# Performance work log

Measured on AMD Instinct MI355X. Metric: run time of the kernel, lower is better.

Reference implementation:

```python
import jax, jax.numpy as jnp
import numpy as np

B, C, H, W = 8, 256, 64, 64
EPS = 1e-5


def _mk_conv_bn(key, oc, ic):
    k = jax.random.split(key, 6)
    return dict(
        w=jax.random.normal(k[0], (oc, ic), jnp.float32) * 0.01,  # trunc-normal approx, stddev 0.01
        b=jnp.zeros((oc,), jnp.float32),
        s=jax.random.uniform(k[1], (oc,), jnp.float32, 0.5, 1.5),   # BN scale
        t=jax.random.normal(k[2], (oc,), jnp.float32) * 0.1,        # BN shift
        m=jax.random.normal(k[3], (oc,), jnp.float32) * 0.1,        # BN running mean
        v=jax.random.uniform(k[4], (oc,), jnp.float32, 0.5, 1.5),   # BN running var
    )


def setup_inputs() -> dict:
    key = jax.random.key(0)
    ks = jax.random.split(key, 6)
    d = {"x": jax.random.normal(ks[0], (B, C, H, W), jnp.float32)}
    for i, (oc, ic) in zip([1, 2, 3, 4], [(C // 8, C), (C // 8, C), (C // 2, C), (C, C // 2)]):
        p = _mk_conv_bn(ks[i], oc, ic)
        for name, val in p.items():
            d[f"{name}{i}"] = val
    d["gamma"] = jnp.asarray(0.5, jnp.float32)
    return d


def _cbn(x, w, b, s, t, m, v, relu=True):
    # conv1x1 + BatchNorm(eval) [+ ReLU]; dropout is identity at inference
    y = jnp.einsum('bchw,oc->bohw', x, w) + b[None, :, None, None]
    scale = (s / jnp.sqrt(v + EPS))[None, :, None, None]
    y = (y - m[None, :, None, None]) * scale + t[None, :, None, None]
    return jax.nn.relu(y) if relu else y


def _maxpool2(x):
    b, c, h, w = x.shape
    return x.reshape(b, c, h // 2, 2, w // 2, 2).max(axis=(3, 5))


def reference(x, w1, b1, s1, t1, m1, v1, w2, b2, s2, t2, m2, v2,
              w3, b3, s3, t3, m3, v3, w4, b4, s4, t4, m4, v4, gamma):
    b, c, h, w = x.shape
    f = _maxpool2(_cbn(x, w1, b1, s1, t1, m1, v1))   # (B, C/8, H/2, W/2)
    g = _cbn(x, w2, b2, s2, t2, m2, v2)              # (B, C/8, H, W)
    hh = _maxpool2(_cbn(x, w3, b3, s3, t3, m3, v3))  # (B, C/2, H/2, W/2)
    hw, hw4 = h * w, (h // 2) * (w // 2)
    f = f.reshape(b, c // 8, hw4).transpose(0, 2, 1)  # (B, HW/4, C/8)
    g = g.reshape(b, c // 8, hw)                      # (B, C/8, HW)
    s = jnp.einsum('bnk,bkm->bnm', f, g)              # (B, HW/4, HW)
    beta = jax.nn.softmax(s, axis=1)                  # softmax over dim=1, as in source
    hh = hh.reshape(b, c // 2, hw4)                   # (B, C/2, HW/4)
    o = jnp.einsum('bcn,bnm->bcm', hh, beta).reshape(b, c // 2, h, w)
    out = _cbn(o, w4, b4, s4, t4, m4, v4, relu=False)
    return gamma * out + x
```

## Files before the change

kernel.cpp:

```cpp
#include <hip/hip_runtime.h>
#include <hip/hip_bf16.h>

#define HW   4096
#define HW4  1024
#define EPS  1e-5f

typedef __attribute__((ext_vector_type(8))) short bf16x8;
typedef __attribute__((ext_vector_type(4))) float f32x4;

__device__ __forceinline__ short f2bs(float f) {
    union { float f; unsigned u; } v; v.f = f;
    unsigned r = v.u + 0x7FFFu + ((v.u >> 16) & 1u);
    return (short)(r >> 16);
}
__device__ __forceinline__ float bs2f(short s) {
    union { unsigned u; float f; } v; v.u = ((unsigned)(unsigned short)s) << 16;
    return v.f;
}
__device__ __forceinline__ int swz64(int r, int c) { return (r << 6) + ((c ^ (r & 7)) << 3); }
__device__ __forceinline__ int swz32(int r, int c) { return (r << 5) + ((c ^ (r & 3)) << 3); }

__global__ __launch_bounds__(256) void conv123_mfma(
    const float* __restrict__ x,
    const float* __restrict__ w1, const float* __restrict__ b1, const float* __restrict__ s1,
    const float* __restrict__ t1, const float* __restrict__ m1, const float* __restrict__ v1,
    const float* __restrict__ w2, const float* __restrict__ b2, const float* __restrict__ s2,
    const float* __restrict__ t2, const float* __restrict__ m2, const float* __restrict__ v2,
    const float* __restrict__ w3, const float* __restrict__ b3, const float* __restrict__ s3,
    const float* __restrict__ t3, const float* __restrict__ m3, const float* __restrict__ v3,
    short* __restrict__ y192)
{
    __shared__ __align__(16) short Wl[192 * 64];
    __shared__ __align__(16) short Xl[64 * 64];
    __shared__ float alB[192], beB[192];

    const int t = threadIdx.x;
    const int lane = t & 63, wv = t >> 6;
    const int quad = lane >> 4, l16 = lane & 15;
    const int bz = blockIdx.y;
    const int pBase = blockIdx.x * 64;

    if (t < 192) {
        int j = t;
        float pb, ps, ptv, pm, pv;
        if (j < 32)      { pb = b1[j]; ps = s1[j]; ptv = t1[j]; pm = m1[j]; pv = v1[j]; }
        else if (j < 64) { int c = j - 32; pb = b2[c]; ps = s2[c]; ptv = t2[c]; pm = m2[c]; pv = v2[c]; }
        else             { int c = j - 64; pb = b3[c]; ps = s3[c]; ptv = t3[c]; pm = m3[c]; pv = v3[c]; }
        float al = ps * rsqrtf(pv + EPS);
        alB[j] = al; beB[j] = (pb - pm) * al + ptv;
    }

    const f32x4 fzero = {0.f, 0.f, 0.f, 0.f};
    f32x4 acc[3][4];
    #pragma unroll
    for (int i = 0; i < 3; ++i)
        #pragma unroll
        for (int j = 0; j < 4; ++j) acc[i][j] = fzero;

    for (int k0 = 0; k0 < 256; k0 += 64) {
        #pragma unroll
        for (int i = 0; i < 3; ++i) {
            int oc = i * 64 + (t >> 2);
            int kb = (t & 3) * 16;
            const float* wp;
            if (oc < 32)      wp = w1 + oc * 256;
            else if (oc < 64) wp = w2 + (oc - 32) * 256;
            else              wp = w3 + (oc - 64) * 256;
            float4 a = *(const float4*)(wp + k0 + kb);
            float4 b = *(const float4*)(wp + k0 + kb + 4);
            float4 c = *(const float4*)(wp + k0 + kb + 8);
            float4 d = *(const float4*)(wp + k0 + kb + 12);
            bf16x8 lo, hi;
            lo[0]=f2bs(a.x); lo[1]=f2bs(a.y); lo[2]=f2bs(a.z); lo[3]=f2bs(a.w);
            lo[4]=f2bs(b.x); lo[5]=f2bs(b.y); lo[6]=f2bs(b.z); lo[7]=f2bs(b.w);
            hi[0]=f2bs(c.x); hi[1]=f2bs(c.y); hi[2]=f2bs(c.z); hi[3]=f2bs(c.w);
            hi[4]=f2bs(d.x); hi[5]=f2bs(d.y); hi[6]=f2bs(d.z); hi[7]=f2bs(d.w);
            *(bf16x8*)&Wl[swz64(oc, (kb >> 3))]     = lo;
            *(bf16x8*)&Wl[swz64(oc, (kb >> 3) + 1)] = hi;
        }
        {
            int pp = t & 63, k8 = t >> 6;
            float fv[16];
            #pragma unroll
            for (int i = 0; i < 16; ++i)
                fv[i] = x[((size_t)bz * 256 + k0 + k8 * 16 + i) * HW + pBase + pp];
            bf16x8 lo, hi;
            #pragma unroll
            for (int i = 0; i < 8; ++i) { lo[i] = f2bs(fv[i]); hi[i] = f2bs(fv[8 + i]); }
            *(bf16x8*)&Xl[swz64(pp, k8 * 2)]     = lo;
            *(bf16x8*)&Xl[swz64(pp, k8 * 2 + 1)] = hi;
        }
        __syncthreads();
        #pragma unroll
        for (int kk = 0; kk < 2; ++kk) {
            bf16x8 bfr[4];
            #pragma unroll
            for (int pt = 0; pt < 4; ++pt)
                bfr[pt] = *(const bf16x8*)&Xl[swz64(pt * 16 + l16, kk * 4 + quad)];
            #pragma unroll
            for (int tt = 0; tt < 3; ++tt) {
                bf16x8 afr = *(const bf16x8*)&Wl[swz64(wv * 48 + tt * 16 + l16, kk * 4 + quad)];
                #pragma unroll
                for (int pt = 0; pt < 4; ++pt)
                    acc[tt][pt] = __builtin_amdgcn_mfma_f32_16x16x32_bf16(afr, bfr[pt], acc[tt][pt], 0, 0, 0);
            }
        }
        __syncthreads();
    }

    #pragma unroll
    for (int tt = 0; tt < 3; ++tt) {
        #pragma unroll
        for (int r = 0; r < 4; ++r) {
            int oc = wv * 48 + tt * 16 + quad * 4 + r;
            float al = alB[oc], be = beB[oc];
            #pragma unroll
            for (int pt = 0; pt < 4; ++pt) {
                int p = pBase + pt * 16 + l16;
                float y = fmaxf(acc[tt][pt][r] * al + be, 0.f);
                y192[((size_t)bz * 192 + oc) * HW + p] = f2bs(y);
            }
        }
    }
}

__global__ __launch_bounds__(256) void pool_kernel(
    const short* __restrict__ y192, short* __restrict__ fbuf, short* __restrict__ hhbuf)
{
    int t  = blockIdx.x * 256 + threadIdx.x;
    int n  = t & 1023;
    int ch = (t >> 10) % 160;
    int bz = t / (1024 * 160);
    int ph = n >> 5, pw = n & 31;
    int j = (ch < 32) ? ch : (ch + 32);
    const short* src = y192 + ((size_t)bz * 192 + j) * HW + (ph * 2) * 64 + pw * 2;
    float v00 = bs2f(src[0]), v01 = bs2f(src[1]), v10 = bs2f(src[64]), v11 = bs2f(src[65]);
    float mx = fmaxf(fmaxf(v00, v01), fmaxf(v10, v11));
    short o = f2bs(mx);
    if (ch < 32) fbuf[((size_t)bz * 32 + ch) * HW4 + n]          = o;
    else         hhbuf[((size_t)bz * 128 + (ch - 32)) * HW4 + n] = o;
}

__global__ __launch_bounds__(256) void attn_mfma(
    const short* __restrict__ y192,
    const short* __restrict__ fbuf,
    const short* __restrict__ hhbuf,
    short* __restrict__ obuf)
{
    __shared__ __align__(16) short gTl[64 * 32];
    __shared__ __align__(16) short fTl[64 * 32];
    __shared__ __align__(16) short hhl[128 * 64];
    __shared__ __align__(16) short sTl[64 * 64];

    const int t = threadIdx.x;
    const int lane = t & 63, wv = t >> 6;
    const int quad = lane >> 4, l16 = lane & 15;
    const int bz = blockIdx.y;
    const int m0 = blockIdx.x * 64;
    const int ms = wv * 16;
    const f32x4 fzero = {0.f, 0.f, 0.f, 0.f};

    {
        int mm = t & 63, k8 = t >> 6;
        bf16x8 v;
        #pragma unroll
        for (int j = 0; j < 8; ++j)
            v[j] = y192[((size_t)bz * 192 + 32 + k8 * 8 + j) * HW + m0 + mm];
        *(bf16x8*)&gTl[swz32(mm, k8)] = v;
    }
    __syncthreads();
    bf16x8 bg = *(const bf16x8*)&gTl[swz32(ms + l16, quad)];

    float runmax = -1e30f, runsum = 0.f;
    f32x4 oacc[8];
    #pragma unroll
    for (int i = 0; i < 8; ++i) oacc[i] = fzero;

    for (int n0 = 0; n0 < 1024; n0 += 64) {
        __syncthreads();
        {
            int nn = t & 63, k8 = t >> 6;
            bf16x8 v;
            #pragma unroll
            for (int j = 0; j < 8; ++j)
                v[j] = fbuf[((size_t)bz * 32 + k8 * 8 + j) * HW4 + n0 + nn];
            *(bf16x8*)&fTl[swz32(nn, k8)] = v;
        }
        {
            int c0 = t >> 3, nc = t & 7;
            #pragma unroll
            for (int i = 0; i < 4; ++i) {
                int c = i * 32 + c0;
                bf16x8 v = *(const bf16x8*)(hhbuf + ((size_t)bz * 128 + c) * HW4 + n0 + nc * 8);
                *(bf16x8*)&hhl[swz64(c, nc)] = v;
            }
        }
        __syncthreads();

        f32x4 sacc[4];
        #pragma unroll
        for (int nt = 0; nt < 4; ++nt) {
            bf16x8 af = *(const bf16x8*)&fTl[swz32(nt * 16 + l16, quad)];
            sacc[nt] = __builtin_amdgcn_mfma_f32_16x16x32_bf16(af, bg, fzero, 0, 0, 0);
        }

        float tmax = -1e30f;
        #pragma unroll
        for (int nt = 0; nt < 4; ++nt)
            #pragma unroll
            for (int r = 0; r < 4; ++r) tmax = fmaxf(tmax, sacc[nt][r]);
        tmax = fmaxf(tmax, __shfl_xor(tmax, 16));
        tmax = fmaxf(tmax, __shfl_xor(tmax, 32));
        float nmax  = fmaxf(runmax, tmax);
        float alpha = __expf(runmax - nmax);
        float psum = 0.f;
        #pragma unroll
        for (int nt = 0; nt < 4; ++nt) {
            short4 ev;
            #pragma unroll
            for (int r = 0; r < 4; ++r) {
                float e = __expf(sacc[nt][r] - nmax);
                psum += e;
                ((short*)&ev)[r] = f2bs(e);
            }
            int chunk = nt * 2 + (quad >> 1);
            *(short4*)&sTl[swz64(ms + l16, chunk) + (quad & 1) * 4] = ev;
        }
        psum += __shfl_xor(psum, 16);
        psum += __shfl_xor(psum, 32);
        runsum = runsum * alpha + psum;
        runmax = nmax;

        #pragma unroll
        for (int ct = 0; ct < 8; ++ct) oacc[ct] = oacc[ct] * alpha;
        #pragma unroll
        for (int kk = 0; kk < 2; ++kk) {
            bf16x8 bs = *(const bf16x8*)&sTl[swz64(ms + l16, kk * 4 + quad)];
            #pragma unroll
            for (int ct = 0; ct < 8; ++ct) {
                bf16x8 ah = *(const bf16x8*)&hhl[swz64(ct * 16 + l16, kk * 4 + quad)];
                oacc[ct] = __builtin_amdgcn_mfma_f32_16x16x32_bf16(ah, bs, oacc[ct], 0, 0, 0);
            }
        }
    }

    float inv = 1.0f / runsum;
    int m = m0 + ms + l16;
    #pragma unroll
    for (int ct = 0; ct < 8; ++ct) {
        short4 ov;
        #pragma unroll
        for (int r = 0; r < 4; ++r) ((short*)&ov)[r] = f2bs(oacc[ct][r] * inv);
        *(short4*)(obuf + ((size_t)bz * HW + m) * 128 + ct * 16 + quad * 4) = ov;
    }
}

__global__ __launch_bounds__(256) void conv4_mfma(
    const short* __restrict__ obuf,
    const float* __restrict__ x,
    const float* __restrict__ w4, const float* __restrict__ b4, const float* __restrict__ s4,
    const float* __restrict__ t4, const float* __restrict__ m4, const float* __restrict__ v4,
    const float* __restrict__ gamma, float* __restrict__ out)
{
    __shared__ __align__(16) short Wl[256 * 64];
    __shared__ __align__(16) short Xl[64 * 64];
    __shared__ float alB[256], beB[256];

    const int t = threadIdx.x;
    const int lane = t & 63, wv = t >> 6;
    const int quad = lane >> 4, l16 = lane & 15;
    const int bz = blockIdx.y;
    const int pBase = blockIdx.x * 64;

    {
        float al = s4[t] * rsqrtf(v4[t] + EPS);
        alB[t] = al; beB[t] = (b4[t] - m4[t]) * al + t4[t];
    }

    const f32x4 fzero = {0.f, 0.f, 0.f, 0.f};
    f32x4 acc[4][4];
    #pragma unroll
    for (int i = 0; i < 4; ++i)
        #pragma unroll
        for (int j = 0; j < 4; ++j) acc[i][j] = fzero;

    for (int k0 = 0; k0 < 128; k0 += 64) {
        #pragma unroll
        for (int i = 0; i < 4; ++i) {
            int oc = i * 64 + (t >> 2);
            int kb = (t & 3) * 16;
            const float* wp = w4 + oc * 128 + k0 + kb;
            float4 a = *(const float4*)(wp);
            float4 b = *(const float4*)(wp + 4);
            float4 c = *(const float4*)(wp + 8);
            float4 d = *(const float4*)(wp + 12);
            bf16x8 lo, hi;
            lo[0]=f2bs(a.x); lo[1]=f2bs(a.y); lo[2]=f2bs(a.z); lo[3]=f2bs(a.w);
            lo[4]=f2bs(b.x); lo[5]=f2bs(b.y); lo[6]=f2bs(b.z); lo[7]=f2bs(b.w);
            hi[0]=f2bs(c.x); hi[1]=f2bs(c.y); hi[2]=f2bs(c.z); hi[3]=f2bs(c.w);
            hi[4]=f2bs(d.x); hi[5]=f2bs(d.y); hi[6]=f2bs(d.z); hi[7]=f2bs(d.w);
            *(bf16x8*)&Wl[swz64(oc, (kb >> 3))]     = lo;
            *(bf16x8*)&Wl[swz64(oc, (kb >> 3) + 1)] = hi;
        }
        {
            int pp = t >> 2, cb = (t & 3) * 16;
            const short* op = obuf + ((size_t)bz * HW + pBase + pp) * 128 + k0 + cb;
            bf16x8 lo = *(const bf16x8*)op;
            bf16x8 hi = *(const bf16x8*)(op + 8);
            *(bf16x8*)&Xl[swz64(pp, cb >> 3)]       = lo;
            *(bf16x8*)&Xl[swz64(pp, (cb >> 3) + 1)] = hi;
        }
        __syncthreads();
        #pragma unroll
        for (int kk = 0; kk < 2; ++kk) {
            bf16x8 bfr[4];
            #pragma unroll
            for (int pt = 0; pt < 4; ++pt)
                bfr[pt] = *(const bf16x8*)&Xl[swz64(pt * 16 + l16, kk * 4 + quad)];
            #pragma unroll
            for (int ot = 0; ot < 4; ++ot) {
                bf16x8 af = *(const bf16x8*)&Wl[swz64(wv * 64 + ot * 16 + l16, kk * 4 + quad)];
                #pragma unroll
                for (int pt = 0; pt < 4; ++pt)
                    acc[ot][pt] = __builtin_amdgcn_mfma_f32_16x16x32_bf16(af, bfr[pt], acc[ot][pt], 0, 0, 0);
            }
        }
        __syncthreads();
    }

    float gm = gamma[0];
    #pragma unroll
    for (int ot = 0; ot < 4; ++ot) {
        #pragma unroll
        for (int r = 0; r < 4; ++r) {
            int oc = wv * 64 + ot * 16 + quad * 4 + r;
            float al = alB[oc], be = beB[oc];
            #pragma unroll
            for (int pt = 0; pt < 4; ++pt) {
                int p = pBase + pt * 16 + l16;
                float y  = acc[ot][pt][r] * al + be;
                float xo = x[((size_t)bz * 256 + oc) * HW + p];
                out[((size_t)bz * 256 + oc) * HW + p] = gm * y + xo;
            }
        }
    }
}

extern "C" void kernel_launch(void* const* d_in, const int* in_sizes, int n_in,
                              void* d_out, int out_size, void* d_ws, size_t ws_size,
                              hipStream_t stream)
{
    const float* x  = (const float*)d_in[0];
    const float* w1 = (const float*)d_in[1];
    const float* b1 = (const float*)d_in[2];
    const float* s1 = (const float*)d_in[3];
    const float* t1 = (const float*)d_in[4];
    const float* m1 = (const float*)d_in[5];
    const float* v1 = (const float*)d_in[6];
    const float* w2 = (const float*)d_in[7];
    const float* b2 = (const float*)d_in[8];
    const float* s2 = (const float*)d_in[9];
    const float* t2 = (const float*)d_in[10];
    const float* m2 = (const float*)d_in[11];
    const float* v2 = (const float*)d_in[12];
    const float* w3 = (const float*)d_in[13];
    const float* b3 = (const float*)d_in[14];
    const float* s3 = (const float*)d_in[15];
    const float* t3 = (const float*)d_in[16];
    const float* m3 = (const float*)d_in[17];
    const float* v3 = (const float*)d_in[18];
    const float* w4 = (const float*)d_in[19];
    const float* b4 = (const float*)d_in[20];
    const float* s4 = (const float*)d_in[21];
    const float* t4 = (const float*)d_in[22];
    const float* m4 = (const float*)d_in[23];
    const float* v4 = (const float*)d_in[24];
    const float* gm = (const float*)d_in[25];
    float* out = (float*)d_out;

    short* y192  = (short*)d_ws;
    short* fbuf  = y192  + (size_t)8 * 192 * 4096;
    short* hhbuf = fbuf  + (size_t)8 * 32 * 1024;
    short* obuf  = hhbuf + (size_t)8 * 128 * 1024;

    conv123_mfma<<<dim3(64, 8), 256, 0, stream>>>(
        x, w1, b1, s1, t1, m1, v1, w2, b2, s2, t2, m2, v2, w3, b3, s3, t3, m3, v3, y192);
    pool_kernel<<<dim3(5120), 256, 0, stream>>>(y192, fbuf, hhbuf);
    attn_mfma<<<dim3(64, 8), 256, 0, stream>>>(y192, fbuf, hhbuf, obuf);
    conv4_mfma<<<dim3(64, 8), 256, 0, stream>>>(
        obuf, x, w4, b4, s4, t4, m4, v4, gm, out);
}
```

Baseline: 184.7 us.

## Fuse maxpool into conv123 epilogue and conv4 into attention kernel

The conv1/2/3 kernel is re-tiled to 128 pixels (two image rows) by 64 output channels per block, so 2x2 max-pooling happens in the epilogue via register max and lane shuffles. This drops the separate pool kernel and the full 192-channel intermediate; only g is written at full resolution. The attention kernel now keeps its normalized output tile in shared memory and runs the conv4 GEMM plus residual directly, removing the obuf round trip and one launch. In exchange, each conv block reloads x for each of three output-channel tiles, and the fused attention kernel uses more shared memory, which may lower occupancy.

```diff
diff --git a/kernel.cpp b/kernel.cpp
--- a/kernel.cpp
+++ b/kernel.cpp
@@ -13,14 +13,11 @@
     unsigned r = v.u + 0x7FFFu + ((v.u >> 16) & 1u);
     return (short)(r >> 16);
 }
-__device__ __forceinline__ float bs2f(short s) {
-    union { unsigned u; float f; } v; v.u = ((unsigned)(unsigned short)s) << 16;
-    return v.f;
-}
-__device__ __forceinline__ int swz64(int r, int c) { return (r << 6) + ((c ^ (r & 7)) << 3); }
-__device__ __forceinline__ int swz32(int r, int c) { return (r << 5) + ((c ^ (r & 3)) << 3); }
-
-__global__ __launch_bounds__(256) void conv123_mfma(
+__device__ __forceinline__ int swz64(int r, int c)  { return (r << 6) + ((c ^ (r & 7))  << 3); }
+__device__ __forceinline__ int swz32(int r, int c)  { return (r << 5) + ((c ^ (r & 3))  << 3); }
+__device__ __forceinline__ int swz128(int r, int c) { return (r << 7) + ((c ^ (r & 15)) << 3); }
+
+__global__ __launch_bounds__(256) void conv123pool(
     const float* __restrict__ x,
     const float* __restrict__ w1, const float* __restrict__ b1, const float* __restrict__ s1,
     const float* __restrict__ t1, const float* __restrict__ m1, const float* __restrict__ v1,
@@ -28,268 +25,45 @@
     const float* __restrict__ t2, const float* __restrict__ m2, const float* __restrict__ v2,
     const float* __restrict__ w3, const float* __restrict__ b3, const float* __restrict__ s3,
     const float* __restrict__ t3, const float* __restrict__ m3, const float* __restrict__ v3,
-    short* __restrict__ y192)
+    short* __restrict__ gbuf, short* __restrict__ fbuf, short* __restrict__ hhbuf)
 {
-    __shared__ __align__(16) short Wl[192 * 64];
-    __shared__ __align__(16) short Xl[64 * 64];
-    __shared__ float alB[192], beB[192];
+    __shared__ __align__(16) short Wl[64 * 64];
+    __shared__ __align__(16) short Xl[128 * 64];
+    __shared__ float alB[64], beB[64];
 
     const int t = threadIdx.x;
     const int lane = t & 63, wv = t >> 6;
     const int quad = lane >> 4, l16 = lane & 15;
-    const int bz = blockIdx.y;
-    const int pBase = blockIdx.x * 64;
-
-    if (t < 192) {
-        int j = t;
+    const int ptile = blockIdx.x;
+    const int octile = blockIdx.y;
+    const int bz = blockIdx.z;
+    const int pBase = ptile * 128;
+
+    if (t < 64) {
+        int j = octile * 64 + t;
         float pb, ps, ptv, pm, pv;
         if (j < 32)      { pb = b1[j]; ps = s1[j]; ptv = t1[j]; pm = m1[j]; pv = v1[j]; }
         else if (j < 64) { int c = j - 32; pb = b2[c]; ps = s2[c]; ptv = t2[c]; pm = m2[c]; pv = v2[c]; }
         else             { int c = j - 64; pb = b3[c]; ps = s3[c]; ptv = t3[c]; pm = m3[c]; pv = v3[c]; }
         float al = ps * rsqrtf(pv + EPS);
-        alB[j] = al; beB[j] = (pb - pm) * al + ptv;
+        alB[t] = al; beB[t] = (pb - pm) * al + ptv;
     }
 
     const f32x4 fzero = {0.f, 0.f, 0.f, 0.f};
-    f32x4 acc[3][4];
-    #pragma unroll
-    for (int i = 0; i < 3; ++i)
-        #pragma unroll
-        for (int j = 0; j < 4; ++j) acc[i][j] = fzero;
+    f32x4 acc[8];
+    #pragma unroll
+    for (int i = 0; i < 8; ++i) acc[i] = fzero;
+
+    const int woc = t >> 2, wkb = (t & 3) * 16;
+    const int xp  = t & 127, xk8 = t >> 7;
 
     for (int k0 = 0; k0 < 256; k0 += 64) {
-        #pragma unroll
-        for (int i = 0; i < 3; ++i) {
-            int oc = i * 64 + (t >> 2);
-            int kb = (t & 3) * 16;
-            const float* wp;
-            if (oc < 32)      wp = w1 + oc * 256;
-            else if (oc < 64) wp = w2 + (oc - 32) * 256;
-            else              wp = w3 + (oc - 64) * 256;
-            float4 a = *(const float4*)(wp + k0 + kb);
-            float4 b = *(const float4*)(wp + k0 + kb + 4);
-            float4 c = *(const float4*)(wp + k0 + kb + 8);
-            float4 d = *(const float4*)(wp + k0 + kb + 12);
-            bf16x8 lo, hi;
-            lo[0]=f2bs(a.x); lo[1]=f2bs(a.y); lo[2]=f2bs(a.z); lo[3]=f2bs(a.w);
-            lo[4]=f2bs(b.x); lo[5]=f2bs(b.y); lo[6]=f2bs(b.z); lo[7]=f2bs(b.w);
-            hi[0]=f2bs(c.x); hi[1]=f2bs(c.y); hi[2]=f2bs(c.z); hi[3]=f2bs(c.w);
-            hi[4]=f2bs(d.x); hi[5]=f2bs(d.y); hi[6]=f2bs(d.z); hi[7]=f2bs(d.w);
-            *(bf16x8*)&Wl[swz64(oc, (kb >> 3))]     = lo;
-            *(bf16x8*)&Wl[swz64(oc, (kb >> 3) + 1)] = hi;
-        }
         {
-            int pp = t & 63, k8 = t >> 6;
-            float fv[16];
-            #pragma unroll
-            for (int i = 0; i < 16; ++i)
-                fv[i] = x[((size_t)bz * 256 + k0 + k8 * 16 + i) * HW + pBase + pp];
-            bf16x8 lo, hi;
-            #pragma unroll
-            for (int i = 0; i < 8; ++i) { lo[i] = f2bs(fv[i]); hi[i] = f2bs(fv[8 + i]); }
-            *(bf16x8*)&Xl[swz64(pp, k8 * 2)]     = lo;
-            *(bf16x8*)&Xl[swz64(pp, k8 * 2 + 1)] = hi;
-        }
-        __syncthreads();
-        #pragma unroll
-        for (int kk = 0; kk < 2; ++kk) {
-            bf16x8 bfr[4];
-            #pragma unroll
-            for (int pt = 0; pt < 4; ++pt)
-                bfr[pt] = *(const bf16x8*)&Xl[swz64(pt * 16 + l16, kk * 4 + quad)];
-            #pragma unroll
-            for (int tt = 0; tt < 3; ++tt) {
-                bf16x8 afr = *(const bf16x8*)&Wl[swz64(wv * 48 + tt * 16 + l16, kk * 4 + quad)];
-                #pragma unroll
-                for (int pt = 0; pt < 4; ++pt)
-                    acc[tt][pt] = __builtin_amdgcn_mfma_f32_16x16x32_bf16(afr, bfr[pt], acc[tt][pt], 0, 0, 0);
-            }
-        }
-        __syncthreads();
-    }
-
-    #pragma unroll
-    for (int tt = 0; tt < 3; ++tt) {
-        #pragma unroll
-        for (int r = 0; r < 4; ++r) {
-            int oc = wv * 48 + tt * 16 + quad * 4 + r;
-            float al = alB[oc], be = beB[oc];
-            #pragma unroll
-            for (int pt = 0; pt < 4; ++pt) {
-                int p = pBase + pt * 16 + l16;
-                float y = fmaxf(acc[tt][pt][r] * al + be, 0.f);
-                y192[((size_t)bz * 192 + oc) * HW + p] = f2bs(y);
-            }
-        }
-    }
-}
-
-__global__ __launch_bounds__(256) void pool_kernel(
-    const short* __restrict__ y192, short* __restrict__ fbuf, short* __restrict__ hhbuf)
-{
-    int t  = blockIdx.x * 256 + threadIdx.x;
-    int n  = t & 1023;
-    int ch = (t >> 10) % 160;
-    int bz = t / (1024 * 160);
-    int ph = n >> 5, pw = n & 31;
-    int j = (ch < 32) ? ch : (ch + 32);
-    const short* src = y192 + ((size_t)bz * 192 + j) * HW + (ph * 2) * 64 + pw * 2;
-    float v00 = bs2f(src[0]), v01 = bs2f(src[1]), v10 = bs2f(src[64]), v11 = bs2f(src[65]);
-    float mx = fmaxf(fmaxf(v00, v01), fmaxf(v10, v11));
-    short o = f2bs(mx);
-    if (ch < 32) fbuf[((size_t)bz * 32 + ch) * HW4 + n]          = o;
-    else         hhbuf[((size_t)bz * 128 + (ch - 32)) * HW4 + n] = o;
-}
-
-__global__ __launch_bounds__(256) void attn_mfma(
-    const short* __restrict__ y192,
-    const short* __restrict__ fbuf,
-    const short* __restrict__ hhbuf,
-    short* __restrict__ obuf)
-{
-    __shared__ __align__(16) short gTl[64 * 32];
-    __shared__ __align__(16) short fTl[64 * 32];
-    __shared__ __align__(16) short hhl[128 * 64];
-    __shared__ __align__(16) short sTl[64 * 64];
-
-    const int t = threadIdx.x;
-    const int lane = t & 63, wv = t >> 6;
-    const int quad = lane >> 4, l16 = lane & 15;
-    const int bz = blockIdx.y;
-    const int m0 = blockIdx.x * 64;
-    const int ms = wv * 16;
-    const f32x4 fzero = {0.f, 0.f, 0.f, 0.f};
-
-    {
-        int mm = t & 63, k8 = t >> 6;
-        bf16x8 v;
-        #pragma unroll
-        for (int j = 0; j < 8; ++j)
-            v[j] = y192[((size_t)bz * 192 + 32 + k8 * 8 + j) * HW + m0 + mm];
-        *(bf16x8*)&gTl[swz32(mm, k8)] = v;
-    }
-    __syncthreads();
-    bf16x8 bg = *(const bf16x8*)&gTl[swz32(ms + l16, quad)];
-
-    float runmax = -1e30f, runsum = 0.f;
-    f32x4 oacc[8];
-    #pragma unroll
-    for (int i = 0; i < 8; ++i) oacc[i] = fzero;
-
-    for (int n0 = 0; n0 < 1024; n0 += 64) {
-        __syncthreads();
-        {
-            int nn = t & 63, k8 = t >> 6;
-            bf16x8 v;
-            #pragma unroll
-            for (int j = 0; j < 8; ++j)
-                v[j] = fbuf[((size_t)bz * 32 + k8 * 8 + j) * HW4 + n0 + nn];
-            *(bf16x8*)&fTl[swz32(nn, k8)] = v;
-        }
-        {
-            int c0 = t >> 3, nc = t & 7;
-            #pragma unroll
-            for (int i = 0; i < 4; ++i) {
-                int c = i * 32 + c0;
-                bf16x8 v = *(const bf16x8*)(hhbuf + ((size_t)bz * 128 + c) * HW4 + n0 + nc * 8);
-                *(bf16x8*)&hhl[swz64(c, nc)] = v;
-            }
-        }
-        __syncthreads();
-
-        f32x4 sacc[4];
-        #pragma unroll
-        for (int nt = 0; nt < 4; ++nt) {
-            bf16x8 af = *(const bf16x8*)&fTl[swz32(nt * 16 + l16, quad)];
-            sacc[nt] = __builtin_amdgcn_mfma_f32_16x16x32_bf16(af, bg, fzero, 0, 0, 0);
-        }
-
-        float tmax = -1e30f;
-        #pragma unroll
-        for (int nt = 0; nt < 4; ++nt)
-            #pragma unroll
-            for (int r = 0; r < 4; ++r) tmax = fmaxf(tmax, sacc[nt][r]);
-        tmax = fmaxf(tmax, __shfl_xor(tmax, 16));
-        tmax = fmaxf(tmax, __shfl_xor(tmax, 32));
-        float nmax  = fmaxf(runmax, tmax);
-        float alpha = __expf(runmax - nmax);
-        float psum = 0.f;
-        #pragma unroll
-        for (int nt = 0; nt < 4; ++nt) {
-            short4 ev;
-            #pragma unroll
-            for (int r = 0; r < 4; ++r) {
-                float e = __expf(sacc[nt][r] - nmax);
-                psum += e;
-                ((short*)&ev)[r] = f2bs(e);
-            }
-            int chunk = nt * 2 + (quad >> 1);
-            *(short4*)&sTl[swz64(ms + l16, chunk) + (quad & 1) * 4] = ev;
-        }
-        psum += __shfl_xor(psum, 16);
-        psum += __shfl_xor(psum, 32);
-        runsum = runsum * alpha + psum;
-        runmax = nmax;
-
-        #pragma unroll
-        for (int ct = 0; ct < 8; ++ct) oacc[ct] = oacc[ct] * alpha;
-        #pragma unroll
-        for (int kk = 0; kk < 2; ++kk) {
-            bf16x8 bs = *(const bf16x8*)&sTl[swz64(ms + l16, kk * 4 + quad)];
-            #pragma unroll
-            for (int ct = 0; ct < 8; ++ct) {
-                bf16x8 ah = *(const bf16x8*)&hhl[swz64(ct * 16 + l16, kk * 4 + quad)];
-                oacc[ct] = __builtin_amdgcn_mfma_f32_16x16x32_bf16(ah, bs, oacc[ct], 0, 0, 0);
-            }
-        }
-    }
-
-    float inv = 1.0f / runsum;
-    int m = m0 + ms + l16;
-    #pragma unroll
-    for (int ct = 0; ct < 8; ++ct) {
-        short4 ov;
-        #pragma unroll
-        for (int r = 0; r < 4; ++r) ((short*)&ov)[r] = f2bs(oacc[ct][r] * inv);
-        *(short4*)(obuf + ((size_t)bz * HW + m) * 128 + ct * 16 + quad * 4) = ov;
-    }
-}
-
-__global__ __launch_bounds__(256) void conv4_mfma(
-    const short* __restrict__ obuf,
-    const float* __restrict__ x,
-    const float* __restrict__ w4, const float* __restrict__ b4, const float* __restrict__ s4,
-    const float* __restrict__ t4, const float* __restrict__ m4, const float* __restrict__ v4,
-    const float* __restrict__ gamma, float* __restrict__ out)
-{
-    __shared__ __align__(16) short Wl[256 * 64];
-    __shared__ __align__(16) short Xl[64 * 64];
-    __shared__ float alB[256], beB[256];
-
-    const int t = threadIdx.x;
-    const int lane = t & 63, wv = t >> 6;
-    const int quad = lane >> 4, l16 = lane & 15;
-    const int bz = blockIdx.y;
-    const int pBase = blockIdx.x * 64;
-
-    {
-        float al = s4[t] * rsqrtf(v4[t] + EPS);
-        alB[t] = al; beB[t] = (b4[t] - m4[t]) * al + t4[t];
-    }
-
-    const f32x4 fzero = {0.f, 0.f, 0.f, 0.f};
-    f32x4 acc[4][4];
-    #pragma unroll
-    for (int i = 0; i < 4; ++i)
-        #pragma unroll
-        for (int j = 0; j < 4; ++j) acc[i][j] = fzero;
-
-    for (int k0 = 0; k0 < 128; k0 += 64) {
-        #pragma unroll
-        for (int i = 0; i < 4; ++i) {
-            int oc = i * 64 + (t >> 2);
-            int kb = (t & 3) * 16;
-            const float* wp = w4 + oc * 128 + k0 + kb;
+            int j = octile * 64 + woc;
+            const float* wp = (j < 32) ? (w1 + j * 256)
+                            : (j < 64) ? (w2 + (j - 32) * 256)
+                                       : (w3 + (j - 64) * 256);
+            wp += k0 + wkb;
             float4 a = *(const float4*)(wp);
             float4 b = *(const float4*)(wp + 4);
             float4 c = *(const float4*)(wp + 8);
@@ -299,30 +73,229 @@
             lo[4]=f2bs(b.x); lo[5]=f2bs(b.y); lo[6]=f2bs(b.z); lo[7]=f2bs(b.w);
             hi[0]=f2bs(c.x); hi[1]=f2bs(c.y); hi[2]=f2bs(c.z); hi[3]=f2bs(c.w);
             hi[4]=f2bs(d.x); hi[5]=f2bs(d.y); hi[6]=f2bs(d.z); hi[7]=f2bs(d.w);
-            *(bf16x8*)&Wl[swz64(oc, (kb >> 3))]     = lo;
-            *(bf16x8*)&Wl[swz64(oc, (kb >> 3) + 1)] = hi;
+            *(bf16x8*)&Wl[swz64(woc, (wkb >> 3))]     = lo;
+            *(bf16x8*)&Wl[swz64(woc, (wkb >> 3) + 1)] = hi;
         }
         {
-            int pp = t >> 2, cb = (t & 3) * 16;
-            const short* op = obuf + ((size_t)bz * HW + pBase + pp) * 128 + k0 + cb;
-            bf16x8 lo = *(const bf16x8*)op;
-            bf16x8 hi = *(const bf16x8*)(op + 8);
-            *(bf16x8*)&Xl[swz64(pp, cb >> 3)]       = lo;
-            *(bf16x8*)&Xl[swz64(pp, (cb >> 3) + 1)] = hi;
+            const float* xp0 = x + ((size_t)bz * 256 + k0 + xk8 * 32) * HW + pBase + xp;
+            float fv[32];
+            #pragma unroll
+            for (int i = 0; i < 32; ++i) fv[i] = xp0[(size_t)i * HW];
+            #pragma unroll
+            for (int c = 0; c < 4; ++c) {
+                bf16x8 v;
+                #pragma unroll
+                for (int jj = 0; jj < 8; ++jj) v[jj] = f2bs(fv[c * 8 + jj]);
+                *(bf16x8*)&Xl[swz64(xp, xk8 * 4 + c)] = v;
+            }
+        }
+        __syncthreads();
+        #pragma unroll
+        for (int kk = 0; kk < 2; ++kk) {
+            bf16x8 afr = *(const bf16x8*)&Wl[swz64(wv * 16 + l16, kk * 4 + quad)];
+            #pragma unroll
+            for (int pt = 0; pt < 8; ++pt) {
+                bf16x8 bfr = *(const bf16x8*)&Xl[swz64(pt * 16 + l16, kk * 4 + quad)];
+                acc[pt] = __builtin_amdgcn_mfma_f32_16x16x32_bf16(afr, bfr, acc[pt], 0, 0, 0);
+            }
+        }
+        __syncthreads();
+    }
+
+    const bool isG = (octile == 0) && (wv >= 2);
+    #pragma unroll
+    for (int r = 0; r < 4; ++r) {
+        int ocl = wv * 16 + quad * 4 + r;
+        float al = alB[ocl], be = beB[ocl];
+        float y[8];
+        #pragma unroll
+        for (int pt = 0; pt < 8; ++pt) y[pt] = fmaxf(acc[pt][r] * al + be, 0.f);
+        int j = octile * 64 + ocl;
+        if (isG) {
+            #pragma unroll
+            for (int pt = 0; pt < 8; ++pt)
+                gbuf[((size_t)bz * 32 + (j - 32)) * HW + pBase + pt * 16 + l16] = f2bs(y[pt]);
+        } else {
+            #pragma unroll
+            for (int pt = 0; pt < 4; ++pt) {
+                float v  = fmaxf(y[pt], y[pt + 4]);
+                float po = fmaxf(v, __shfl_xor(v, 1));
+                if ((l16 & 1) == 0) {
+                    int n = ptile * 32 + ((pt * 16 + l16) >> 1);
+                    if (j < 32) fbuf[((size_t)bz * 32 + j) * HW4 + n] = f2bs(po);
+                    else        hhbuf[((size_t)bz * 128 + (j - 64)) * HW4 + n] = f2bs(po);
+                }
+            }
+        }
+    }
+}
+
+__global__ __launch_bounds__(256) void attn_conv4(
+    const short* __restrict__ gbuf,
+    const short* __restrict__ fbuf,
+    const short* __restrict__ hhbuf,
+    const float* __restrict__ x,
+    const float* __restrict__ w4, const float* __restrict__ b4, const float* __restrict__ s4,
+    const float* __restrict__ t4, const float* __restrict__ m4, const float* __restrict__ v4,
+    const float* __restrict__ gamma, float* __restrict__ out)
+{
+    __shared__ __align__(16) short smem[24576];
+    __shared__ float alB4[256], beB4[256];
+    short* gTl = smem;
+    short* fTl = smem + 2048;
+    short* sTl = smem + 4096;
+    short* hhl = smem + 8192;
+    short* o_l = smem;
+    short* Wl4 = smem + 8192;
+
+    const int t = threadIdx.x;
+    const int lane = t & 63, wv = t >> 6;
+    const int quad = lane >> 4, l16 = lane & 15;
+    const int bz = blockIdx.y;
+    const int m0 = blockIdx.x * 64;
+    const int ms = wv * 16;
+    const f32x4 fzero = {0.f, 0.f, 0.f, 0.f};
+
+    {
+        float al = s4[t] * rsqrtf(v4[t] + EPS);
+        alB4[t] = al; beB4[t] = (b4[t] - m4[t]) * al + t4[t];
+    }
+
+    {
+        int mm = t & 63, k8 = t >> 6;
+        bf16x8 v;
+        #pragma unroll
+        for (int j = 0; j < 8; ++j)
+            v[j] = gbuf[((size_t)bz * 32 + k8 * 8 + j) * HW + m0 + mm];
+        *(bf16x8*)&gTl[swz32(mm, k8)] = v;
+    }
+    __syncthreads();
+    bf16x8 bg = *(const bf16x8*)&gTl[swz32(ms + l16, quad)];
+
+    float runmax = -1e30f, runsum = 0.f;
+    f32x4 oacc[8];
+    #pragma unroll
+    for (int i = 0; i < 8; ++i) oacc[i] = fzero;
+
+    for (int n0 = 0; n0 < 1024; n0 += 64) {
+        __syncthreads();
+        {
+            int nn = t & 63, k8 = t >> 6;
+            bf16x8 v;
+            #pragma unroll
+            for (int j = 0; j < 8; ++j)
+                v[j] = fbuf[((size_t)bz * 32 + k8 * 8 + j) * HW4 + n0 + nn];
+            *(bf16x8*)&fTl[swz32(nn, k8)] = v;
+        }
+        {
+            int c0 = t >> 3, nc = t & 7;
+            #pragma unroll
+            for (int i = 0; i < 4; ++i) {
+                int c = i * 32 + c0;
+                bf16x8 v = *(const bf16x8*)(hhbuf + ((size_t)bz * 128 + c) * HW4 + n0 + nc * 8);
+                *(bf16x8*)&hhl[swz64(c, nc)] = v;
+            }
+        }
+        __syncthreads();
+
+        f32x4 sacc[4];
+        #pragma unroll
+        for (int nt = 0; nt < 4; ++nt) {
+            bf16x8 af = *(const bf16x8*)&fTl[swz32(nt * 16 + l16, quad)];
+            sacc[nt] = __builtin_amdgcn_mfma_f32_16x16x32_bf16(af, bg, fzero, 0, 0, 0);
+        }
+
+        float tmax = -1e30f;
+        #pragma unroll
+        for (int nt = 0; nt < 4; ++nt)
+            #pragma unroll
+            for (int r = 0; r < 4; ++r) tmax = fmaxf(tmax, sacc[nt][r]);
+        tmax = fmaxf(tmax, __shfl_xor(tmax, 16));
+        tmax = fmaxf(tmax, __shfl_xor(tmax, 32));
+        float nmax  = fmaxf(runmax, tmax);
+        float alpha = __expf(runmax - nmax);
+        float psum = 0.f;
+        #pragma unroll
+        for (int nt = 0; nt < 4; ++nt) {
+            short4 ev;
+            #pragma unroll
+            for (int r = 0; r < 4; ++r) {
+                float e = __expf(sacc[nt][r] - nmax);
+                psum += e;
+                ((short*)&ev)[r] = f2bs(e);
+            }
+            int chunk = nt * 2 + (quad >> 1);
+            *(short4*)&sTl[swz64(ms + l16, chunk) + (quad & 1) * 4] = ev;
+        }
+        psum += __shfl_xor(psum, 16);
+        psum += __shfl_xor(psum, 32);
+        runsum = runsum * alpha + psum;
+        runmax = nmax;
+
+        #pragma unroll
+        for (int ct = 0; ct < 8; ++ct) oacc[ct] = oacc[ct] * alpha;
+        #pragma unroll
+        for (int kk = 0; kk < 2; ++kk) {
+            bf16x8 bs = *(const bf16x8*)&sTl[swz64(ms + l16, kk * 4 + quad)];
+            #pragma unroll
+            for (int ct = 0; ct < 8; ++ct) {
+                bf16x8 ah = *(const bf16x8*)&hhl[swz64(ct * 16 + l16, kk * 4 + quad)];
+                oacc[ct] = __builtin_amdgcn_mfma_f32_16x16x32_bf16(ah, bs, oacc[ct], 0, 0, 0);
+            }
+        }
+    }
+    __syncthreads();
+
+    {
+        float inv = 1.0f / runsum;
+        int m = ms + l16;
+        #pragma unroll
+        for (int ct = 0; ct < 8; ++ct) {
+            short4 ov;
+            #pragma unroll
+            for (int r = 0; r < 4; ++r) ((short*)&ov)[r] = f2bs(oacc[ct][r] * inv);
+            *(short4*)&o_l[swz128(m, ct * 2 + (quad >> 1)) + (quad & 1) * 4] = ov;
+        }
+    }
+    __syncthreads();
+
+    f32x4 acc4[4][4];
+    #pragma unroll
+    for (int i = 0; i < 4; ++i)
+        #pragma unroll
+        for (int j = 0; j < 4; ++j) acc4[i][j] = fzero;
+
+    for (int c0 = 0; c0 < 128; c0 += 64) {
+        #pragma unroll
+        for (int i = 0; i < 4; ++i) {
+            int oc = i * 64 + (t >> 2);
+            int kb = (t & 3) * 16;
+            const float* wp = w4 + oc * 128 + c0 + kb;
+            float4 a = *(const float4*)(wp);
+            float4 b = *(const float4*)(wp + 4);
+            float4 c = *(const float4*)(wp + 8);
+            float4 d = *(const float4*)(wp + 12);
+            bf16x8 lo, hi;
+            lo[0]=f2bs(a.x); lo[1]=f2bs(a.y); lo[2]=f2bs(a.z); lo[3]=f2bs(a.w);
+            lo[4]=f2bs(b.x); lo[5]=f2bs(b.y); lo[6]=f2bs(b.z); lo[7]=f2bs(b.w);
+            hi[0]=f2bs(c.x); hi[1]=f2bs(c.y); hi[2]=f2bs(c.z); hi[3]=f2bs(c.w);
+            hi[4]=f2bs(d.x); hi[5]=f2bs(d.y); hi[6]=f2bs(d.z); hi[7]=f2bs(d.w);
+            *(bf16x8*)&Wl4[swz64(oc, (kb >> 3))]     = lo;
+            *(bf16x8*)&Wl4[swz64(oc, (kb >> 3) + 1)] = hi;
         }
         __syncthreads();
         #pragma unroll
         for (int kk = 0; kk < 2; ++kk) {
             bf16x8 bfr[4];
             #pragma unroll
-            for (int pt = 0; pt < 4; ++pt)
-                bfr[pt] = *(const bf16x8*)&Xl[swz64(pt * 16 + l16, kk * 4 + quad)];
+            for (int mt = 0; mt < 4; ++mt)
+                bfr[mt] = *(const bf16x8*)&o_l[swz128(mt * 16 + l16, (c0 >> 3) + kk * 4 + quad)];
             #pragma unroll
             for (int ot = 0; ot < 4; ++ot) {
-                bf16x8 af = *(const bf16x8*)&Wl[swz64(wv * 64 + ot * 16 + l16, kk * 4 + quad)];
+                bf16x8 afr = *(const bf16x8*)&Wl4[swz64(wv * 64 + ot * 16 + l16, kk * 4 + quad)];
                 #pragma unroll
-                for (int pt = 0; pt < 4; ++pt)
-                    acc[ot][pt] = __builtin_amdgcn_mfma_f32_16x16x32_bf16(af, bfr[pt], acc[ot][pt], 0, 0, 0);
+                for (int mt = 0; mt < 4; ++mt)
+                    acc4[ot][mt] = __builtin_amdgcn_mfma_f32_16x16x32_bf16(afr, bfr[mt], acc4[ot][mt], 0, 0, 0);
             }
         }
         __syncthreads();
@@ -334,11 +307,11 @@
         #pragma unroll
         for (int r = 0; r < 4; ++r) {
             int oc = wv * 64 + ot * 16 + quad * 4 + r;
-            float al = alB[oc], be = beB[oc];
-            #pragma unroll
-            for (int pt = 0; pt < 4; ++pt) {
-                int p = pBase + pt * 16 + l16;
-                float y  = acc[ot][pt][r] * al + be;
+            float al = alB4[oc], be = beB4[oc];
+            #pragma unroll
+            for (int mt = 0; mt < 4; ++mt) {
+                int p = m0 + mt * 16 + l16;
+                float y  = acc4[ot][mt][r] * al + be;
                 float xo = x[((size_t)bz * 256 + oc) * HW + p];
                 out[((size_t)bz * 256 + oc) * HW + p] = gm * y + xo;
             }
@@ -378,15 +351,13 @@
     const float* gm = (const float*)d_in[25];
     float* out = (float*)d_out;
 
-    short* y192  = (short*)d_ws;
-    short* fbuf  = y192  + (size_t)8 * 192 * 4096;
+    short* gbuf  = (short*)d_ws;
+    short* fbuf  = gbuf  + (size_t)8 * 32 * 4096;
     short* hhbuf = fbuf  + (size_t)8 * 32 * 1024;
-    short* obuf  = hhbuf + (size_t)8 * 128 * 1024;
-
-    conv123_mfma<<<dim3(64, 8), 256, 0, stream>>>(
-        x, w1, b1, s1, t1, m1, v1, w2, b2, s2, t2, m2, v2, w3, b3, s3, t3, m3, v3, y192);
-    pool_kernel<<<dim3(5120), 256, 0, stream>>>(y192, fbuf, hhbuf);
-    attn_mfma<<<dim3(64, 8), 256, 0, stream>>>(y192, fbuf, hhbuf, obuf);
-    conv4_mfma<<<dim3(64, 8), 256, 0, stream>>>(
-        obuf, x, w4, b4, s4, t4, m4, v4, gm, out);
+
+    conv123pool<<<dim3(32, 3, 8), 256, 0, stream>>>(
+        x, w1, b1, s1, t1, m1, v1, w2, b2, s2, t2, m2, v2, w3, b3, s3, t3, m3, v3,
+        gbuf, fbuf, hhbuf);
+    attn_conv4<<<dim3(64, 8), 256, 0, stream>>>(
+        gbuf, fbuf, hhbuf, x, w4, b4, s4, t4, m4, v4, gm, out);
 }
```

After: 173.9 us. 5.8% less time.
